# Optimization experiments

Measured on AMD Instinct MI355X. Metric: run time of the kernel, lower is better.

## Reference

```python
import jax, jax.numpy as jnp
import numpy as np


def setup_inputs() -> dict:
    key = jax.random.key(0)
    B, F, K = 8192, 8192, 64
    x = jax.random.normal(key, (B, F), dtype=jnp.float32)
    weight = jnp.ones((F,), dtype=jnp.float32)
    return {"x": x, "weight": weight, "k": K}


def reference(x, weight, k):
    # x: [B, F], weight: [F]
    xw = x * weight
    # torch code detaches before topk; mask is a constant w.r.t. grads
    xv = jax.lax.stop_gradient(xw)
    _, idx_top = jax.lax.top_k(xv, k)    # [B, k] indices of k largest
    _, idx_bot = jax.lax.top_k(-xv, k)   # [B, k] indices of k smallest
    rows = jnp.arange(xw.shape[0])[:, None]  # [B, 1]
    z = jnp.ones_like(xw)
    z = z.at[rows, idx_top].set(0.0)
    z = z.at[rows, idx_bot].set(0.0)
    return xw * z
```

## Files before the change

kernel.cpp:

```cpp
#include <hip/hip_runtime.h>
#include <stdint.h>

#define ROWLEN 8192
#define KSEL 64
#define NT 256
#define VPT 8
#define NH 8
#define HPAD 264
#define MAXEQ 256

__device__ __forceinline__ uint32_t f2key(float f) {
    uint32_t u = __float_as_uint(f);
    return (u & 0x80000000u) ? ~u : (u | 0x80000000u);
}
__device__ __forceinline__ float key2f(uint32_t k) {
    uint32_t u = (k & 0x80000000u) ? (k ^ 0x80000000u) : ~k;
    return __uint_as_float(u);
}

struct SelOut { uint32_t bin, k, cnt; };

__device__ __forceinline__ SelOut select256(uint32_t cnt, uint32_t S, uint32_t kcur,
                                            uint32_t* wsum, uint32_t* bc,
                                            int tid, int lane, int wid) {
    uint32_t p = cnt;
    #pragma unroll
    for (int d = 1; d < 64; d <<= 1) {
        uint32_t y = __shfl_up(p, (unsigned)d, 64);
        if (lane >= d) p += y;
    }
    if (lane == 63) wsum[wid] = p;
    __syncthreads();
    uint32_t off = 0;
    #pragma unroll
    for (int w = 0; w < 4; ++w) if (w < wid) off += wsum[w];
    p += off;
    uint32_t target = S - kcur + 1u;
    if (p >= target && (p - cnt) < target) {
        bc[0] = (uint32_t)tid;
        bc[1] = kcur - (S - p);
        bc[2] = cnt;
    }
    __syncthreads();
    SelOut o; o.bin = bc[0]; o.k = bc[1]; o.cnt = bc[2];
    return o;
}

extern "C" __global__ void __launch_bounds__(NT, 4)
topk_mask_kernel(const float* __restrict__ x, const float* __restrict__ w,
                 float* __restrict__ out) {
    __shared__ uint32_t hist8[NH][HPAD];
    __shared__ uint32_t hist[256];
    __shared__ uint32_t wsum[4];
    __shared__ uint32_t bc[3];
    __shared__ uint32_t eqidx[MAXEQ];
    __shared__ uint32_t s_ec;
    __shared__ int s_cut;

    const int tid  = threadIdx.x;
    const int lane = tid & 63;
    const int wid  = tid >> 6;
    const int hcopy = (wid << 1) | (lane & 1);
    const size_t row = blockIdx.x;

    const float4* xr = (const float4*)(x + row * (size_t)ROWLEN);
    const float4* wr = (const float4*)w;

    uint32_t key[VPT][4];
    #pragma unroll
    for (int j = 0; j < VPT; ++j) {
        float4 a = xr[j * NT + tid];
        float4 b = wr[j * NT + tid];
        key[j][0] = f2key(a.x * b.x);
        key[j][1] = f2key(a.y * b.y);
        key[j][2] = f2key(a.z * b.z);
        key[j][3] = f2key(a.w * b.w);
    }

    for (int i = tid; i < NH * HPAD; i += NT) ((uint32_t*)hist8)[i] = 0;
    __syncthreads();
    #pragma unroll
    for (int j = 0; j < VPT; ++j)
        #pragma unroll
        for (int c = 0; c < 4; ++c)
            atomicAdd(&hist8[hcopy][key[j][c] >> 24], 1u);
    __syncthreads();

    uint32_t Tkey[2];
    int cutv[2];

    for (int pass = 0; pass < 2; ++pass) {
        uint32_t mb = pass ? (255u - (uint32_t)tid) : (uint32_t)tid;
        uint32_t cnt = 0;
        #pragma unroll
        for (int h = 0; h < NH; ++h) cnt += hist8[h][mb];
        SelOut s = select256(cnt, ROWLEN, KSEL, wsum, bc, tid, lane, wid);
        uint32_t prefix = s.bin << 24;
        uint32_t kcur = s.k, S = s.cnt;

        for (int shift = 16; shift >= 0; shift -= 8) {
            hist[tid] = 0;
            __syncthreads();
            #pragma unroll
            for (int j = 0; j < VPT; ++j)
                #pragma unroll
                for (int c = 0; c < 4; ++c) {
                    uint32_t tk = pass ? ~key[j][c] : key[j][c];
                    if (((tk ^ prefix) >> (shift + 8)) == 0u)
                        atomicAdd(&hist[(tk >> shift) & 0xFFu], 1u);
                }
            __syncthreads();
            s = select256(hist[tid], S, kcur, wsum, bc, tid, lane, wid);
            prefix |= s.bin << shift;
            kcur = s.k;
            S = s.cnt;
        }

        if (tid == 0) { s_ec = 0; s_cut = 0x7FFFFFFF; }
        __syncthreads();
        #pragma unroll
        for (int j = 0; j < VPT; ++j)
            #pragma unroll
            for (int c = 0; c < 4; ++c) {
                uint32_t tk = pass ? ~key[j][c] : key[j][c];
                if (tk == prefix) {
                    uint32_t pos = atomicAdd(&s_ec, 1u);
                    if (pos < MAXEQ) eqidx[pos] = (uint32_t)((j * NT + tid) * 4 + c);
                }
            }
        __syncthreads();
        uint32_t ec = s_ec;
        int cut;
        if (ec <= MAXEQ) {
            if ((uint32_t)tid < ec) {
                uint32_t my = eqidx[tid];
                uint32_t rank = 0;
                for (uint32_t j2 = 0; j2 < ec; ++j2)
                    rank += (eqidx[j2] < my) ? 1u : 0u;
                if (rank + 1u == kcur) s_cut = (int)my;
            }
            __syncthreads();
            cut = s_cut;
        } else {
            cut = 0x7FFFFFFF;
        }
        Tkey[pass] = prefix;
        cutv[pass] = cut;
        __syncthreads();
    }

    const uint32_t Thi = Tkey[0], Tlo = Tkey[1];
    const int cutHi = cutv[0], cutLo = cutv[1];

    float4* orow = (float4*)(out + row * (size_t)ROWLEN);
    #pragma unroll
    for (int j = 0; j < VPT; ++j) {
        float f[4];
        #pragma unroll
        for (int c = 0; c < 4; ++c) {
            uint32_t kh = key[j][c];
            uint32_t kl = ~kh;
            int idx = (j * NT + tid) * 4 + c;
            bool z = (kh > Thi) || (kh == Thi && idx <= cutHi) ||
                     (kl > Tlo) || (kl == Tlo && idx <= cutLo);
            f[c] = z ? 0.0f : key2f(kh);
        }
        orow[j * NT + tid] = make_float4(f[0], f[1], f[2], f[3]);
    }
}

extern "C" void kernel_launch(void* const* d_in, const int* in_sizes, int n_in,
                              void* d_out, int out_size, void* d_ws, size_t ws_size,
                              hipStream_t stream) {
    const float* x = (const float*)d_in[0];
    const float* w = (const float*)d_in[1];
    float* out = (float*)d_out;
    const int rows = out_size / ROWLEN;
    topk_mask_kernel<<<dim3(rows), dim3(NT), 0, stream>>>(x, w, out);
}
```

Baseline: 489.2 us.

## Compact boundary-bin candidates into shared lists for radix refinement; nontemporal output stores

After the first 8-bit histogram pass, elements that fall in the selected top and bottom bins are compacted into shared-memory lists, provided each bin holds at most 512 entries. The later radix refinement passes and the tie-resolution step then scan only these short lists instead of all 32 register-held keys per thread. The output is written with nontemporal stores. In exchange the kernel uses more LDS, which may lower occupancy, and it adds an extra compaction pass with atomics.

```diff
diff --git a/kernel.cpp b/kernel.cpp
--- a/kernel.cpp
+++ b/kernel.cpp
@@ -7,7 +7,9 @@
 #define VPT 8
 #define NH 8
 #define HPAD 264
-#define MAXEQ 256
+#define CAP 512
+
+typedef float f32x4 __attribute__((ext_vector_type(4)));
 
 __device__ __forceinline__ uint32_t f2key(float f) {
     uint32_t u = __float_as_uint(f);
@@ -53,9 +55,12 @@
     __shared__ uint32_t hist[256];
     __shared__ uint32_t wsum[4];
     __shared__ uint32_t bc[3];
-    __shared__ uint32_t eqidx[MAXEQ];
+    __shared__ uint32_t eqidx[CAP];
     __shared__ uint32_t s_ec;
     __shared__ int s_cut;
+    __shared__ uint32_t listKey[2][CAP];
+    __shared__ uint16_t listIdx[2][CAP];
+    __shared__ uint32_t listCnt[2];
 
     const int tid  = threadIdx.x;
     const int lane = tid & 63;
@@ -86,54 +91,105 @@
             atomicAdd(&hist8[hcopy][key[j][c] >> 24], 1u);
     __syncthreads();
 
-    uint32_t Tkey[2];
-    int cutv[2];
-
+    SelOut sel1[2];
     for (int pass = 0; pass < 2; ++pass) {
         uint32_t mb = pass ? (255u - (uint32_t)tid) : (uint32_t)tid;
         uint32_t cnt = 0;
         #pragma unroll
         for (int h = 0; h < NH; ++h) cnt += hist8[h][mb];
-        SelOut s = select256(cnt, ROWLEN, KSEL, wsum, bc, tid, lane, wid);
-        uint32_t prefix = s.bin << 24;
-        uint32_t kcur = s.k, S = s.cnt;
+        sel1[pass] = select256(cnt, ROWLEN, KSEL, wsum, bc, tid, lane, wid);
+    }
+
+    const bool useL0 = sel1[0].cnt <= CAP;
+    const bool useL1 = sel1[1].cnt <= CAP;
+    const uint32_t bRawHi = sel1[0].bin;
+    const uint32_t bRawLo = 255u - sel1[1].bin;
+    if (tid < 2) listCnt[tid] = 0;
+    __syncthreads();
+    if (useL0 || useL1) {
+        #pragma unroll
+        for (int j = 0; j < VPT; ++j)
+            #pragma unroll
+            for (int c = 0; c < 4; ++c) {
+                uint32_t kk = key[j][c];
+                uint32_t b = kk >> 24;
+                uint32_t idx = (uint32_t)((j * NT + tid) * 4 + c);
+                if (useL0 && b == bRawHi) {
+                    uint32_t pos = atomicAdd(&listCnt[0], 1u);
+                    listKey[0][pos] = kk;
+                    listIdx[0][pos] = (uint16_t)idx;
+                }
+                if (useL1 && b == bRawLo) {
+                    uint32_t pos = atomicAdd(&listCnt[1], 1u);
+                    listKey[1][pos] = ~kk;
+                    listIdx[1][pos] = (uint16_t)idx;
+                }
+            }
+    }
+    __syncthreads();
+
+    uint32_t Tkey[2];
+    int cutv[2];
+
+    for (int pass = 0; pass < 2; ++pass) {
+        uint32_t prefix = sel1[pass].bin << 24;
+        uint32_t kcur = sel1[pass].k, S = sel1[pass].cnt;
+        const bool ul = pass ? useL1 : useL0;
+        const uint32_t lc = listCnt[pass];
 
         for (int shift = 16; shift >= 0; shift -= 8) {
             hist[tid] = 0;
             __syncthreads();
+            if (ul) {
+                for (uint32_t i = (uint32_t)tid; i < lc; i += NT) {
+                    uint32_t tk = listKey[pass][i];
+                    if (((tk ^ prefix) >> (shift + 8)) == 0u)
+                        atomicAdd(&hist[(tk >> shift) & 0xFFu], 1u);
+                }
+            } else {
+                #pragma unroll
+                for (int j = 0; j < VPT; ++j)
+                    #pragma unroll
+                    for (int c = 0; c < 4; ++c) {
+                        uint32_t tk = pass ? ~key[j][c] : key[j][c];
+                        if (((tk ^ prefix) >> (shift + 8)) == 0u)
+                            atomicAdd(&hist[(tk >> shift) & 0xFFu], 1u);
+                    }
+            }
+            __syncthreads();
+            SelOut s = select256(hist[tid], S, kcur, wsum, bc, tid, lane, wid);
+            prefix |= s.bin << shift;
+            kcur = s.k;
+            S = s.cnt;
+        }
+
+        if (tid == 0) { s_ec = 0; s_cut = 0x7FFFFFFF; }
+        __syncthreads();
+        if (ul) {
+            for (uint32_t i = (uint32_t)tid; i < lc; i += NT) {
+                if (listKey[pass][i] == prefix) {
+                    uint32_t pos = atomicAdd(&s_ec, 1u);
+                    eqidx[pos] = listIdx[pass][i];
+                }
+            }
+        } else {
             #pragma unroll
             for (int j = 0; j < VPT; ++j)
                 #pragma unroll
                 for (int c = 0; c < 4; ++c) {
                     uint32_t tk = pass ? ~key[j][c] : key[j][c];
-                    if (((tk ^ prefix) >> (shift + 8)) == 0u)
-                        atomicAdd(&hist[(tk >> shift) & 0xFFu], 1u);
-                }
-            __syncthreads();
-            s = select256(hist[tid], S, kcur, wsum, bc, tid, lane, wid);
-            prefix |= s.bin << shift;
-            kcur = s.k;
-            S = s.cnt;
-        }
-
-        if (tid == 0) { s_ec = 0; s_cut = 0x7FFFFFFF; }
-        __syncthreads();
-        #pragma unroll
-        for (int j = 0; j < VPT; ++j)
-            #pragma unroll
-            for (int c = 0; c < 4; ++c) {
-                uint32_t tk = pass ? ~key[j][c] : key[j][c];
-                if (tk == prefix) {
-                    uint32_t pos = atomicAdd(&s_ec, 1u);
-                    if (pos < MAXEQ) eqidx[pos] = (uint32_t)((j * NT + tid) * 4 + c);
-                }
-            }
+                    if (tk == prefix) {
+                        uint32_t pos = atomicAdd(&s_ec, 1u);
+                        if (pos < CAP) eqidx[pos] = (uint32_t)((j * NT + tid) * 4 + c);
+                    }
+                }
+        }
         __syncthreads();
         uint32_t ec = s_ec;
         int cut;
-        if (ec <= MAXEQ) {
-            if ((uint32_t)tid < ec) {
-                uint32_t my = eqidx[tid];
+        if (ec <= CAP) {
+            for (uint32_t i = (uint32_t)tid; i < ec; i += NT) {
+                uint32_t my = eqidx[i];
                 uint32_t rank = 0;
                 for (uint32_t j2 = 0; j2 < ec; ++j2)
                     rank += (eqidx[j2] < my) ? 1u : 0u;
@@ -152,7 +208,7 @@
     const uint32_t Thi = Tkey[0], Tlo = Tkey[1];
     const int cutHi = cutv[0], cutLo = cutv[1];
 
-    float4* orow = (float4*)(out + row * (size_t)ROWLEN);
+    f32x4* orow = (f32x4*)(out + row * (size_t)ROWLEN);
     #pragma unroll
     for (int j = 0; j < VPT; ++j) {
         float f[4];
@@ -165,7 +221,8 @@
                      (kl > Tlo) || (kl == Tlo && idx <= cutLo);
             f[c] = z ? 0.0f : key2f(kh);
         }
-        orow[j * NT + tid] = make_float4(f[0], f[1], f[2], f[3]);
+        f32x4 v = { f[0], f[1], f[2], f[3] };
+        __builtin_nontemporal_store(v, &orow[j * NT + tid]);
     }
 }
 
```

New measurement: 494.6 us. About the same (+1.1%).

## Fuse top/bottom radix selects and compact candidate bins into shared lists

Applied to the files above, without the earlier changes.

Runs the top-k and bottom-k radix selections together, packing both 16-bit prefix scans into one 32-bit shuffle scan so each select round needs a single set of barriers. After the first-digit histogram, when the selected bin holds at most 512 elements, those candidates are compacted into shared-memory lists with a ballot, and the later refinement passes scan only the lists instead of all 32 register keys per thread. The aim is fewer sync rounds and far fewer per-element compare and atomic operations in the refinement passes. The cost is more shared memory, which can lower occupancy, plus the ballot-based compaction step.

```diff
diff --git a/kernel.cpp b/kernel.cpp
--- a/kernel.cpp
+++ b/kernel.cpp
@@ -7,6 +7,7 @@
 #define VPT 8
 #define NH 8
 #define HPAD 264
+#define CAP 512
 #define MAXEQ 256
 
 __device__ __forceinline__ uint32_t f2key(float f) {
@@ -18,12 +19,14 @@
     return __uint_as_float(u);
 }
 
-struct SelOut { uint32_t bin, k, cnt; };
-
-__device__ __forceinline__ SelOut select256(uint32_t cnt, uint32_t S, uint32_t kcur,
-                                            uint32_t* wsum, uint32_t* bc,
-                                            int tid, int lane, int wid) {
-    uint32_t p = cnt;
+struct Sel2 { uint32_t bin0, k0, cnt0, bin1, k1, cnt1; };
+
+__device__ __forceinline__ Sel2 select2(uint32_t c0, uint32_t c1,
+                                        uint32_t S0, uint32_t k0,
+                                        uint32_t S1, uint32_t k1,
+                                        uint32_t* wsum, uint32_t* bc,
+                                        int tid, int lane, int wid) {
+    uint32_t p = c0 | (c1 << 16);
     #pragma unroll
     for (int d = 1; d < 64; d <<= 1) {
         uint32_t y = __shfl_up(p, (unsigned)d, 64);
@@ -35,14 +38,19 @@
     #pragma unroll
     for (int w = 0; w < 4; ++w) if (w < wid) off += wsum[w];
     p += off;
-    uint32_t target = S - kcur + 1u;
-    if (p >= target && (p - cnt) < target) {
-        bc[0] = (uint32_t)tid;
-        bc[1] = kcur - (S - p);
-        bc[2] = cnt;
-    }
-    __syncthreads();
-    SelOut o; o.bin = bc[0]; o.k = bc[1]; o.cnt = bc[2];
+    uint32_t p0 = p & 0xFFFFu, p1 = p >> 16;
+    uint32_t t0 = S0 - k0 + 1u;
+    uint32_t t1 = S1 - k1 + 1u;
+    if (p0 >= t0 && (p0 - c0) < t0) {
+        bc[0] = (uint32_t)tid; bc[1] = k0 - (S0 - p0); bc[2] = c0;
+    }
+    if (p1 >= t1 && (p1 - c1) < t1) {
+        bc[3] = (uint32_t)tid; bc[4] = k1 - (S1 - p1); bc[5] = c1;
+    }
+    __syncthreads();
+    Sel2 o;
+    o.bin0 = bc[0]; o.k0 = bc[1]; o.cnt0 = bc[2];
+    o.bin1 = bc[3]; o.k1 = bc[4]; o.cnt1 = bc[5];
     return o;
 }
 
@@ -50,12 +58,15 @@
 topk_mask_kernel(const float* __restrict__ x, const float* __restrict__ w,
                  float* __restrict__ out) {
     __shared__ uint32_t hist8[NH][HPAD];
-    __shared__ uint32_t hist[256];
+    __shared__ uint32_t hist2[2][256];
     __shared__ uint32_t wsum[4];
-    __shared__ uint32_t bc[3];
-    __shared__ uint32_t eqidx[MAXEQ];
-    __shared__ uint32_t s_ec;
-    __shared__ int s_cut;
+    __shared__ uint32_t bc[6];
+    __shared__ uint32_t eqidx[2][MAXEQ];
+    __shared__ uint32_t s_ec2[2];
+    __shared__ int s_cut2[2];
+    __shared__ uint32_t listKey[2][CAP];
+    __shared__ uint16_t listIdx[2][CAP];
+    __shared__ uint32_t listCnt[2];
 
     const int tid  = threadIdx.x;
     const int lane = tid & 63;
@@ -78,7 +89,10 @@
     }
 
     for (int i = tid; i < NH * HPAD; i += NT) ((uint32_t*)hist8)[i] = 0;
-    __syncthreads();
+    hist2[0][tid] = 0; hist2[1][tid] = 0;
+    if (tid < 2) { listCnt[tid] = 0; s_ec2[tid] = 0; s_cut2[tid] = 0x7FFFFFFF; }
+    __syncthreads();
+
     #pragma unroll
     for (int j = 0; j < VPT; ++j)
         #pragma unroll
@@ -86,71 +100,151 @@
             atomicAdd(&hist8[hcopy][key[j][c] >> 24], 1u);
     __syncthreads();
 
-    uint32_t Tkey[2];
-    int cutv[2];
-
-    for (int pass = 0; pass < 2; ++pass) {
-        uint32_t mb = pass ? (255u - (uint32_t)tid) : (uint32_t)tid;
-        uint32_t cnt = 0;
-        #pragma unroll
-        for (int h = 0; h < NH; ++h) cnt += hist8[h][mb];
-        SelOut s = select256(cnt, ROWLEN, KSEL, wsum, bc, tid, lane, wid);
-        uint32_t prefix = s.bin << 24;
-        uint32_t kcur = s.k, S = s.cnt;
-
-        for (int shift = 16; shift >= 0; shift -= 8) {
-            hist[tid] = 0;
-            __syncthreads();
+    uint32_t c0 = 0, c1 = 0;
+    #pragma unroll
+    for (int h = 0; h < NH; ++h) {
+        c0 += hist8[h][tid];
+        c1 += hist8[h][255 - tid];
+    }
+    Sel2 s1 = select2(c0, c1, ROWLEN, KSEL, ROWLEN, KSEL, wsum, bc, tid, lane, wid);
+    uint32_t pref0 = s1.bin0 << 24, k0 = s1.k0, S0 = s1.cnt0;
+    uint32_t pref1 = s1.bin1 << 24, k1 = s1.k1, S1 = s1.cnt1;
+    const bool ul0 = S0 <= CAP;
+    const bool ul1 = S1 <= CAP;
+    const uint32_t bRawHi = s1.bin0;
+    const uint32_t bRawLo = 255u - s1.bin1;
+
+    if (ul0 || ul1) {
+        #pragma unroll
+        for (int j = 0; j < VPT; ++j)
+            #pragma unroll
+            for (int c = 0; c < 4; ++c) {
+                uint32_t kk = key[j][c];
+                uint32_t b = kk >> 24;
+                bool m0 = ul0 && (b == bRawHi);
+                bool m1 = ul1 && (b == bRawLo);
+                unsigned long long B0 = __ballot(m0);
+                unsigned long long B1 = __ballot(m1);
+                uint32_t idx = (uint32_t)((j * NT + tid) * 4 + c);
+                if (B0) {
+                    uint32_t base = 0;
+                    if (lane == 0) base = atomicAdd(&listCnt[0], (uint32_t)__popcll(B0));
+                    base = __shfl(base, 0, 64);
+                    if (m0) {
+                        uint32_t pos = base + (uint32_t)__popcll(B0 & ((1ull << lane) - 1ull));
+                        listKey[0][pos] = kk;
+                        listIdx[0][pos] = (uint16_t)idx;
+                    }
+                }
+                if (B1) {
+                    uint32_t base = 0;
+                    if (lane == 0) base = atomicAdd(&listCnt[1], (uint32_t)__popcll(B1));
+                    base = __shfl(base, 0, 64);
+                    if (m1) {
+                        uint32_t pos = base + (uint32_t)__popcll(B1 & ((1ull << lane) - 1ull));
+                        listKey[1][pos] = ~kk;
+                        listIdx[1][pos] = (uint16_t)idx;
+                    }
+                }
+            }
+    }
+    __syncthreads();
+    const uint32_t lc0 = listCnt[0], lc1 = listCnt[1];
+
+    for (int shift = 16; shift >= 0; shift -= 8) {
+        if (ul0) {
+            for (uint32_t i = (uint32_t)tid; i < lc0; i += NT) {
+                uint32_t tk = listKey[0][i];
+                if (((tk ^ pref0) >> (shift + 8)) == 0u)
+                    atomicAdd(&hist2[0][(tk >> shift) & 0xFFu], 1u);
+            }
+        } else {
             #pragma unroll
             for (int j = 0; j < VPT; ++j)
                 #pragma unroll
                 for (int c = 0; c < 4; ++c) {
-                    uint32_t tk = pass ? ~key[j][c] : key[j][c];
-                    if (((tk ^ prefix) >> (shift + 8)) == 0u)
-                        atomicAdd(&hist[(tk >> shift) & 0xFFu], 1u);
-                }
-            __syncthreads();
-            s = select256(hist[tid], S, kcur, wsum, bc, tid, lane, wid);
-            prefix |= s.bin << shift;
-            kcur = s.k;
-            S = s.cnt;
-        }
-
-        if (tid == 0) { s_ec = 0; s_cut = 0x7FFFFFFF; }
+                    uint32_t tk = key[j][c];
+                    if (((tk ^ pref0) >> (shift + 8)) == 0u)
+                        atomicAdd(&hist2[0][(tk >> shift) & 0xFFu], 1u);
+                }
+        }
+        if (ul1) {
+            for (uint32_t i = (uint32_t)tid; i < lc1; i += NT) {
+                uint32_t tk = listKey[1][i];
+                if (((tk ^ pref1) >> (shift + 8)) == 0u)
+                    atomicAdd(&hist2[1][(tk >> shift) & 0xFFu], 1u);
+            }
+        } else {
+            #pragma unroll
+            for (int j = 0; j < VPT; ++j)
+                #pragma unroll
+                for (int c = 0; c < 4; ++c) {
+                    uint32_t tk = ~key[j][c];
+                    if (((tk ^ pref1) >> (shift + 8)) == 0u)
+                        atomicAdd(&hist2[1][(tk >> shift) & 0xFFu], 1u);
+                }
+        }
         __syncthreads();
+        uint32_t r0 = hist2[0][tid], r1 = hist2[1][tid];
+        hist2[0][tid] = 0; hist2[1][tid] = 0;
+        Sel2 s = select2(r0, r1, S0, k0, S1, k1, wsum, bc, tid, lane, wid);
+        pref0 |= s.bin0 << shift; k0 = s.k0; S0 = s.cnt0;
+        pref1 |= s.bin1 << shift; k1 = s.k1; S1 = s.cnt1;
+    }
+
+    if (ul0) {
+        for (uint32_t i = (uint32_t)tid; i < lc0; i += NT)
+            if (listKey[0][i] == pref0) {
+                uint32_t pos = atomicAdd(&s_ec2[0], 1u);
+                if (pos < MAXEQ) eqidx[0][pos] = listIdx[0][i];
+            }
+    } else {
         #pragma unroll
         for (int j = 0; j < VPT; ++j)
             #pragma unroll
-            for (int c = 0; c < 4; ++c) {
-                uint32_t tk = pass ? ~key[j][c] : key[j][c];
-                if (tk == prefix) {
-                    uint32_t pos = atomicAdd(&s_ec, 1u);
-                    if (pos < MAXEQ) eqidx[pos] = (uint32_t)((j * NT + tid) * 4 + c);
-                }
-            }
-        __syncthreads();
-        uint32_t ec = s_ec;
-        int cut;
-        if (ec <= MAXEQ) {
-            if ((uint32_t)tid < ec) {
-                uint32_t my = eqidx[tid];
-                uint32_t rank = 0;
-                for (uint32_t j2 = 0; j2 < ec; ++j2)
-                    rank += (eqidx[j2] < my) ? 1u : 0u;
-                if (rank + 1u == kcur) s_cut = (int)my;
-            }
-            __syncthreads();
-            cut = s_cut;
-        } else {
-            cut = 0x7FFFFFFF;
-        }
-        Tkey[pass] = prefix;
-        cutv[pass] = cut;
-        __syncthreads();
-    }
-
-    const uint32_t Thi = Tkey[0], Tlo = Tkey[1];
-    const int cutHi = cutv[0], cutLo = cutv[1];
+            for (int c = 0; c < 4; ++c)
+                if (key[j][c] == pref0) {
+                    uint32_t pos = atomicAdd(&s_ec2[0], 1u);
+                    if (pos < MAXEQ) eqidx[0][pos] = (uint32_t)((j * NT + tid) * 4 + c);
+                }
+    }
+    if (ul1) {
+        for (uint32_t i = (uint32_t)tid; i < lc1; i += NT)
+            if (listKey[1][i] == pref1) {
+                uint32_t pos = atomicAdd(&s_ec2[1], 1u);
+                if (pos < MAXEQ) eqidx[1][pos] = listIdx[1][i];
+            }
+    } else {
+        #pragma unroll
+        for (int j = 0; j < VPT; ++j)
+            #pragma unroll
+            for (int c = 0; c < 4; ++c)
+                if (~key[j][c] == pref1) {
+                    uint32_t pos = atomicAdd(&s_ec2[1], 1u);
+                    if (pos < MAXEQ) eqidx[1][pos] = (uint32_t)((j * NT + tid) * 4 + c);
+                }
+    }
+    __syncthreads();
+    const uint32_t ec0 = s_ec2[0], ec1 = s_ec2[1];
+    if (ec0 <= MAXEQ)
+        for (uint32_t i = (uint32_t)tid; i < ec0; i += NT) {
+            uint32_t my = eqidx[0][i], rank = 0;
+            for (uint32_t j2 = 0; j2 < ec0; ++j2)
+                rank += (eqidx[0][j2] < my) ? 1u : 0u;
+            if (rank + 1u == k0) s_cut2[0] = (int)my;
+        }
+    if (ec1 <= MAXEQ)
+        for (uint32_t i = (uint32_t)tid; i < ec1; i += NT) {
+            uint32_t my = eqidx[1][i], rank = 0;
+            for (uint32_t j2 = 0; j2 < ec1; ++j2)
+                rank += (eqidx[1][j2] < my) ? 1u : 0u;
+            if (rank + 1u == k1) s_cut2[1] = (int)my;
+        }
+    __syncthreads();
+
+    const uint32_t Thi = pref0, Tlo = pref1;
+    const int cutHi = (ec0 <= MAXEQ) ? s_cut2[0] : 0x7FFFFFFF;
+    const int cutLo = (ec1 <= MAXEQ) ? s_cut2[1] : 0x7FFFFFFF;
 
     float4* orow = (float4*)(out + row * (size_t)ROWLEN);
     #pragma unroll
```

Result: slower. 506.7 us (+3.6%).

## Compact candidate bins into shared lists and refine both thresholds with per-wave selection

Applied to the files above, without the earlier changes.

After the first 8-bit histogram, elements falling in the threshold bin for the top and bottom selections are compacted into small shared-memory lists, up to a capacity of 512 each. Two wavefronts then refine the two thresholds in parallel using wave-level histograms, prefix scans and ballots, so each refinement step scans only the candidates instead of all 32 keys per thread. The block-wide barriers used by each pass go away on this path. A fallback keeps the original full-row refinement when a bin overflows the capacity, at the cost of more shared memory (possible occupancy loss) and extra code.

```diff
diff --git a/kernel.cpp b/kernel.cpp
--- a/kernel.cpp
+++ b/kernel.cpp
@@ -7,7 +7,10 @@
 #define VPT 8
 #define NH 8
 #define HPAD 264
+#define CAP 512
 #define MAXEQ 256
+#define HXS 320
+#define HX(b) ((b) + ((b) >> 2))
 
 __device__ __forceinline__ uint32_t f2key(float f) {
     uint32_t u = __float_as_uint(f);
@@ -46,16 +49,54 @@
     return o;
 }
 
+__device__ __forceinline__ void wave_select(const uint32_t c[4], uint32_t S, uint32_t kcur,
+                                            int lane, uint32_t& bin, uint32_t& kloc,
+                                            uint32_t& cnt) {
+    uint32_t t = c[0] + c[1] + c[2] + c[3];
+    uint32_t p = t;
+    #pragma unroll
+    for (int d = 1; d < 64; d <<= 1) {
+        uint32_t y = __shfl_up(p, (unsigned)d, 64);
+        if (lane >= d) p += y;
+    }
+    uint32_t excl = p - t;
+    uint32_t target = S - kcur + 1u;
+    bool cross = (p >= target) && (excl < target);
+    unsigned long long bal = __ballot(cross);
+    uint32_t lbin = 0, lk = 0, lcn = 0;
+    if (cross) {
+        uint32_t cum = excl;
+        #pragma unroll
+        for (int i = 0; i < 4; ++i) {
+            uint32_t nc = cum + c[i];
+            if (cum < target && nc >= target) {
+                lbin = 4u * (uint32_t)lane + (uint32_t)i;
+                lk   = kcur - (S - nc);
+                lcn  = c[i];
+            }
+            cum = nc;
+        }
+    }
+    int src = __ffsll(bal) - 1;
+    bin  = (uint32_t)__shfl((int)lbin, src, 64);
+    kloc = (uint32_t)__shfl((int)lk,  src, 64);
+    cnt  = (uint32_t)__shfl((int)lcn, src, 64);
+}
+
 extern "C" __global__ void __launch_bounds__(NT, 4)
 topk_mask_kernel(const float* __restrict__ x, const float* __restrict__ w,
                  float* __restrict__ out) {
     __shared__ uint32_t hist8[NH][HPAD];
-    __shared__ uint32_t hist[256];
+    __shared__ uint32_t hist2[2][HXS];
     __shared__ uint32_t wsum[4];
     __shared__ uint32_t bc[3];
-    __shared__ uint32_t eqidx[MAXEQ];
-    __shared__ uint32_t s_ec;
-    __shared__ int s_cut;
+    __shared__ uint32_t eqidx[2][MAXEQ];
+    __shared__ uint32_t s_ec, s_cutw;
+    __shared__ uint32_t listKey[2][CAP];
+    __shared__ uint16_t listIdx[2][CAP];
+    __shared__ uint32_t listCnt[2];
+    __shared__ uint32_t r1res[2][3];
+    __shared__ uint32_t fres[2][2];
 
     const int tid  = threadIdx.x;
     const int lane = tid & 63;
@@ -78,7 +119,9 @@
     }
 
     for (int i = tid; i < NH * HPAD; i += NT) ((uint32_t*)hist8)[i] = 0;
-    __syncthreads();
+    if (tid < 2) listCnt[tid] = 0;
+    __syncthreads();
+
     #pragma unroll
     for (int j = 0; j < VPT; ++j)
         #pragma unroll
@@ -86,71 +129,158 @@
             atomicAdd(&hist8[hcopy][key[j][c] >> 24], 1u);
     __syncthreads();
 
-    uint32_t Tkey[2];
-    int cutv[2];
-
-    for (int pass = 0; pass < 2; ++pass) {
-        uint32_t mb = pass ? (255u - (uint32_t)tid) : (uint32_t)tid;
-        uint32_t cnt = 0;
-        #pragma unroll
-        for (int h = 0; h < NH; ++h) cnt += hist8[h][mb];
-        SelOut s = select256(cnt, ROWLEN, KSEL, wsum, bc, tid, lane, wid);
-        uint32_t prefix = s.bin << 24;
-        uint32_t kcur = s.k, S = s.cnt;
-
-        for (int shift = 16; shift >= 0; shift -= 8) {
-            hist[tid] = 0;
+    if (wid < 2) {
+        uint32_t c[4];
+        #pragma unroll
+        for (int i = 0; i < 4; ++i) {
+            uint32_t b  = 4u * (uint32_t)lane + (uint32_t)i;
+            uint32_t rb = wid ? (255u - b) : b;
+            uint32_t s = 0;
+            #pragma unroll
+            for (int h = 0; h < NH; ++h) s += hist8[h][rb];
+            c[i] = s;
+        }
+        uint32_t bin, kloc, cnt;
+        wave_select(c, ROWLEN, KSEL, lane, bin, kloc, cnt);
+        if (lane == 0) { r1res[wid][0] = bin; r1res[wid][1] = kloc; r1res[wid][2] = cnt; }
+    }
+    __syncthreads();
+
+    const uint32_t bin0 = r1res[0][0], k0 = r1res[0][1], S0 = r1res[0][2];
+    const uint32_t bin1 = r1res[1][0], k1 = r1res[1][1], S1 = r1res[1][2];
+    uint32_t Thi, Tlo; int cutHi, cutLo;
+
+    if (S0 > CAP || S1 > CAP) {
+        uint32_t Tk[2]; int cv[2];
+        for (int pass = 0; pass < 2; ++pass) {
+            uint32_t prefix = (pass ? bin1 : bin0) << 24;
+            uint32_t kcur = pass ? k1 : k0, S = pass ? S1 : S0;
+            for (int shift = 16; shift >= 0; shift -= 8) {
+                hist2[0][tid] = 0;
+                __syncthreads();
+                #pragma unroll
+                for (int j = 0; j < VPT; ++j)
+                    #pragma unroll
+                    for (int c = 0; c < 4; ++c) {
+                        uint32_t tk = pass ? ~key[j][c] : key[j][c];
+                        if (((tk ^ prefix) >> (shift + 8)) == 0u)
+                            atomicAdd(&hist2[0][(tk >> shift) & 0xFFu], 1u);
+                    }
+                __syncthreads();
+                SelOut s = select256(hist2[0][tid], S, kcur, wsum, bc, tid, lane, wid);
+                prefix |= s.bin << shift; kcur = s.k; S = s.cnt;
+            }
+            if (tid == 0) { s_ec = 0; s_cutw = 0x7FFFFFFFu; }
             __syncthreads();
             #pragma unroll
             for (int j = 0; j < VPT; ++j)
                 #pragma unroll
                 for (int c = 0; c < 4; ++c) {
                     uint32_t tk = pass ? ~key[j][c] : key[j][c];
-                    if (((tk ^ prefix) >> (shift + 8)) == 0u)
-                        atomicAdd(&hist[(tk >> shift) & 0xFFu], 1u);
+                    if (tk == prefix) {
+                        uint32_t pos = atomicAdd(&s_ec, 1u);
+                        if (pos < MAXEQ) eqidx[0][pos] = (uint32_t)((j * NT + tid) * 4 + c);
+                    }
                 }
             __syncthreads();
-            s = select256(hist[tid], S, kcur, wsum, bc, tid, lane, wid);
-            prefix |= s.bin << shift;
-            kcur = s.k;
-            S = s.cnt;
-        }
-
-        if (tid == 0) { s_ec = 0; s_cut = 0x7FFFFFFF; }
-        __syncthreads();
+            uint32_t ec = s_ec; int cut;
+            if (ec <= MAXEQ) {
+                if ((uint32_t)tid < ec) {
+                    uint32_t my = eqidx[0][tid], rank = 0;
+                    for (uint32_t j2 = 0; j2 < ec; ++j2)
+                        rank += (eqidx[0][j2] < my) ? 1u : 0u;
+                    if (rank + 1u == kcur) s_cutw = my;
+                }
+                __syncthreads();
+                cut = (int)s_cutw;
+            } else cut = 0x7FFFFFFF;
+            Tk[pass] = prefix; cv[pass] = cut;
+            __syncthreads();
+        }
+        Thi = Tk[0]; Tlo = Tk[1]; cutHi = cv[0]; cutLo = cv[1];
+    } else {
+        const uint32_t bRawHi = bin0, bRawLo = 255u - bin1;
         #pragma unroll
         for (int j = 0; j < VPT; ++j)
             #pragma unroll
             for (int c = 0; c < 4; ++c) {
-                uint32_t tk = pass ? ~key[j][c] : key[j][c];
-                if (tk == prefix) {
-                    uint32_t pos = atomicAdd(&s_ec, 1u);
-                    if (pos < MAXEQ) eqidx[pos] = (uint32_t)((j * NT + tid) * 4 + c);
+                uint32_t kk = key[j][c];
+                uint32_t b = kk >> 24;
+                uint32_t idx = (uint32_t)((j * NT + tid) * 4 + c);
+                if (b == bRawHi) {
+                    uint32_t pos = atomicAdd(&listCnt[0], 1u);
+                    listKey[0][pos] = kk;
+                    listIdx[0][pos] = (uint16_t)idx;
+                }
+                if (b == bRawLo) {
+                    uint32_t pos = atomicAdd(&listCnt[1], 1u);
+                    listKey[1][pos] = ~kk;
+                    listIdx[1][pos] = (uint16_t)idx;
                 }
             }
         __syncthreads();
-        uint32_t ec = s_ec;
-        int cut;
-        if (ec <= MAXEQ) {
-            if ((uint32_t)tid < ec) {
-                uint32_t my = eqidx[tid];
-                uint32_t rank = 0;
-                for (uint32_t j2 = 0; j2 < ec; ++j2)
-                    rank += (eqidx[j2] < my) ? 1u : 0u;
-                if (rank + 1u == kcur) s_cut = (int)my;
-            }
-            __syncthreads();
-            cut = s_cut;
-        } else {
-            cut = 0x7FFFFFFF;
-        }
-        Tkey[pass] = prefix;
-        cutv[pass] = cut;
+
+        if (wid < 2) {
+            const int p = wid;
+            const uint32_t lc = listCnt[p];
+            uint32_t* h = hist2[p];
+            const uint32_t* lk = listKey[p];
+            const uint16_t* li = listIdx[p];
+            uint32_t prefix = (p ? bin1 : bin0) << 24;
+            uint32_t kcur = p ? k1 : k0, S = p ? S1 : S0;
+
+            for (int shift = 16; shift >= 0; shift -= 8) {
+                #pragma unroll
+                for (int i = 0; i < 4; ++i) h[HX(4u * (uint32_t)lane + i)] = 0;
+                __builtin_amdgcn_wave_barrier();
+                for (uint32_t i = (uint32_t)lane; i < lc; i += 64) {
+                    uint32_t tk = lk[i];
+                    if (((tk ^ prefix) >> (shift + 8)) == 0u)
+                        atomicAdd(&h[HX((tk >> shift) & 0xFFu)], 1u);
+                }
+                __builtin_amdgcn_wave_barrier();
+                uint32_t c[4];
+                #pragma unroll
+                for (int i = 0; i < 4; ++i) c[i] = h[HX(4u * (uint32_t)lane + i)];
+                uint32_t bin, kloc, cnt;
+                wave_select(c, S, kcur, lane, bin, kloc, cnt);
+                prefix |= bin << shift; kcur = kloc; S = cnt;
+            }
+
+            uint32_t* eq = eqidx[p];
+            uint32_t ec = 0;
+            for (uint32_t base = 0; base < lc; base += 64) {
+                uint32_t i = base + (uint32_t)lane;
+                bool m = (i < lc) && (lk[i] == prefix);
+                unsigned long long bal = __ballot(m);
+                if (m) {
+                    uint32_t pos = ec + (uint32_t)__popcll(bal & ((1ull << lane) - 1ull));
+                    if (pos < MAXEQ) eq[pos] = li[i];
+                }
+                ec += (uint32_t)__popcll(bal);
+            }
+            __builtin_amdgcn_wave_barrier();
+            int cut = 0x7FFFFFFF;
+            if (ec <= MAXEQ) {
+                uint32_t fcut = 0xFFFFFFFFu;
+                for (uint32_t i = (uint32_t)lane; i < ec; i += 64) {
+                    uint32_t my = eq[i], rank = 0;
+                    for (uint32_t j2 = 0; j2 < ec; ++j2)
+                        rank += (eq[j2] < my) ? 1u : 0u;
+                    if (rank + 1u == kcur) fcut = my;
+                }
+                unsigned long long bal = __ballot(fcut != 0xFFFFFFFFu);
+                if (bal) {
+                    int src = __ffsll(bal) - 1;
+                    cut = __shfl((int)fcut, src, 64);
+                }
+            }
+            if (lane == 0) { fres[p][0] = prefix; fres[p][1] = (uint32_t)cut; }
+        }
         __syncthreads();
-    }
-
-    const uint32_t Thi = Tkey[0], Tlo = Tkey[1];
-    const int cutHi = cutv[0], cutLo = cutv[1];
+        Thi = fres[0][0]; cutHi = (int)fres[0][1];
+        Tlo = fres[1][0]; cutLo = (int)fres[1][1];
+    }
 
     float4* orow = (float4*)(out + row * (size_t)ROWLEN);
     #pragma unroll
```

Result: faster. 474.3 us (-3.1%).
